# Kernel optimization log

Measured on AMD Instinct MI355X. Metric: run time of the kernel, lower is better.

Reference implementation:

```python
import jax, jax.numpy as jnp
import numpy as np

SCALE = 1.0 / np.sqrt(64.0)  # module hardcodes 64**0.5, independent of d


def setup_inputs() -> dict:
    key = jax.random.key(0)
    k1, k2 = jax.random.split(key)
    x = jax.random.normal(k1, (8, 2048, 512), dtype=jnp.float32)
    kernel = jax.random.normal(k2, (3, 512, 512), dtype=jnp.float32) * 0.02
    return {"x": x, "kernel": kernel}


def reference(x, kernel):
    # x: [b, s, d]; kernel: [3, d, d]
    q = jnp.einsum('bsd,de->bse', x, kernel[0])
    k = jnp.einsum('bsd,de->bse', x, kernel[1])
    v = jnp.einsum('bsd,de->bse', x, kernel[2])
    scores = jnp.einsum('bqd,bkd->bqk', q, k) * SCALE  # [b, s, s]
    attn = jax.nn.softmax(scores, axis=-1)
    return jnp.einsum('bqk,bkd->bqd', attn, v)
```

## Files before the change

### kernel.cpp

```cpp
#include <hip/hip_runtime.h>


typedef unsigned short u16;
typedef unsigned int u32;

using bf16x8 = __attribute__((ext_vector_type(8))) short;
using f32x4  = __attribute__((ext_vector_type(4))) float;
using u16x4  = __attribute__((ext_vector_type(4))) u16;

__device__ __forceinline__ u16 f2bf(float f) {
  u32 u = __float_as_uint(f);
  u32 r = (u + 0x7FFFu + ((u >> 16) & 1u)) >> 16;
  return (u16)r;
}
__device__ __forceinline__ float bf2f(u16 h) {
  return __uint_as_float(((u32)h) << 16);
}

#define GLL16(src, dst)                                                        \
  __builtin_amdgcn_global_load_lds(                                            \
      (const __attribute__((address_space(1))) void*)(src),                    \
      (__attribute__((address_space(3))) void*)(dst), 16, 0, 0)

template <int K>
__device__ __forceinline__ void gemm8p_256x128(
    const u16* __restrict__ A0, const u16* __restrict__ B0,
    u16* lds, f32x4 (&acc)[4][4])
{
  const int tid = threadIdx.x;
  const int w = tid >> 6, l = tid & 63;
  const int wm = w >> 1, wn = w & 1;
  const int fr = l & 15;
  const int laneChunk = ((l >> 4) ^ ((fr >> 1) & 3)) << 3;
  const int laneA = (wm * 64 + fr) * 32 + laneChunk;
  const int laneB = (wn * 64 + fr) * 32 + laneChunk;
  u16* const ldsA = lds;
  u16* const ldsB = lds + 24576;

  const int chunkS = ((tid & 3) ^ ((tid >> 3) & 3)) << 3;
  const int r0 = tid >> 2;
  const u16* const sA0 = A0 + (size_t)r0 * K + chunkS;
  const u16* const sA1 = A0 + (size_t)(r0 + 128) * K + chunkS;
  const u16* const sB0 = B0 + (size_t)r0 * K + chunkS;
  const int dOf = w * 512;

#define PSTAGE_A(j, slot) do {                                                 \
    u16* d_ = ldsA + (slot) * 8192 + dOf;                                      \
    GLL16(sA0 + (j) * 32, d_);                                                 \
    GLL16(sA1 + (j) * 32, d_ + 4096);                                          \
  } while (0)
#define PSTAGE_B(j, slot) do {                                                 \
    u16* d_ = ldsB + (slot) * 4096 + dOf;                                      \
    GLL16(sB0 + (j) * 32, d_);                                                 \
  } while (0)

  PSTAGE_B(0, 0); PSTAGE_A(0, 0);
  PSTAGE_B(1, 1); PSTAGE_A(1, 1);

  constexpr int NS = K / 32;
  int slot = 0;
  for (int j = 0; j < NS; ++j) {
    const int jn = (j + 2 < NS) ? (j + 2) : (NS - 1);
    int slotn = slot + 2; if (slotn >= 3) slotn -= 3;

    asm volatile("s_waitcnt vmcnt(3)\n\ts_barrier" ::: "memory");

    const u16* const Ab = ldsA + slot * 8192;
    const u16* const Bb = ldsB + slot * 4096;
    bf16x8 a[4], b[4];
#pragma unroll
    for (int i = 0; i < 4; ++i) a[i] = *(const bf16x8*)(Ab + laneA + i * 512);
#pragma unroll
    for (int i = 0; i < 4; ++i) b[i] = *(const bf16x8*)(Bb + laneB + i * 512);
    PSTAGE_B(jn, slotn);
    __builtin_amdgcn_s_setprio(1);
#pragma unroll
    for (int mi = 0; mi < 2; ++mi)
#pragma unroll
      for (int nj = 0; nj < 4; ++nj)
        acc[mi][nj] = __builtin_amdgcn_mfma_f32_16x16x32_bf16(a[mi], b[nj], acc[mi][nj], 0, 0, 0);
    __builtin_amdgcn_s_setprio(0);
    PSTAGE_A(jn, slotn);
    __builtin_amdgcn_s_setprio(1);
#pragma unroll
    for (int mi = 2; mi < 4; ++mi)
#pragma unroll
      for (int nj = 0; nj < 4; ++nj)
        acc[mi][nj] = __builtin_amdgcn_mfma_f32_16x16x32_bf16(a[mi], b[nj], acc[mi][nj], 0, 0, 0);
    __builtin_amdgcn_s_setprio(0);

    slot = (slot == 2) ? 0 : slot + 1;
  }
#undef PSTAGE_A
#undef PSTAGE_B
}

template <int K>
__device__ __forceinline__ void gemm8p_256sq(
    const u16* __restrict__ A0, const u16* __restrict__ B0,
    u16* lds, f32x4 (&acc)[8][4])
{
  const int tid = threadIdx.x;
  const int w = tid >> 6, l = tid & 63;
  const int wm = w >> 2, wn = w & 3;
  const int fr = l & 15;
  const int laneChunk = ((l >> 4) ^ ((fr >> 1) & 3)) << 3;
  const int laneA = (wm * 128 + fr) * 32 + laneChunk;
  const int laneB = (wn * 64 + fr) * 32 + laneChunk;
  u16* const ldsA = lds;
  u16* const ldsB = lds + 24576;

  const int chunkS = ((tid & 3) ^ ((tid >> 3) & 3)) << 3;
  const int r0 = tid >> 2;
  const u16* const sA0 = A0 + (size_t)r0 * K + chunkS;
  const u16* const sA1 = A0 + (size_t)(r0 + 128) * K + chunkS;
  const u16* const sB0 = B0 + (size_t)r0 * K + chunkS;
  const u16* const sB1 = B0 + (size_t)(r0 + 128) * K + chunkS;
  const int dOf = w * 512;

#define SSTAGE_A(j, slot) do {                                                 \
    u16* d_ = ldsA + (slot) * 8192 + dOf;                                      \
    GLL16(sA0 + (j) * 32, d_);                                                 \
    GLL16(sA1 + (j) * 32, d_ + 4096);                                          \
  } while (0)
#define SSTAGE_B(j, slot) do {                                                 \
    u16* d_ = ldsB + (slot) * 8192 + dOf;                                      \
    GLL16(sB0 + (j) * 32, d_);                                                 \
    GLL16(sB1 + (j) * 32, d_ + 4096);                                          \
  } while (0)

  SSTAGE_B(0, 0); SSTAGE_A(0, 0);
  SSTAGE_B(1, 1); SSTAGE_A(1, 1);

  constexpr int NS = K / 32;
  int slot = 0;
  for (int j = 0; j < NS; ++j) {
    const int jn = (j + 2 < NS) ? (j + 2) : (NS - 1);
    int slotn = slot + 2; if (slotn >= 3) slotn -= 3;

    asm volatile("s_waitcnt vmcnt(4)\n\ts_barrier" ::: "memory");

    const u16* const Ab = ldsA + slot * 8192;
    const u16* const Bb = ldsB + slot * 8192;
    bf16x8 b[4], a0[4], a1[4];
#pragma unroll
    for (int i = 0; i < 4; ++i) b[i]  = *(const bf16x8*)(Bb + laneB + i * 512);
#pragma unroll
    for (int i = 0; i < 4; ++i) a0[i] = *(const bf16x8*)(Ab + laneA + i * 512);
    SSTAGE_A(jn, slotn);
    __builtin_amdgcn_s_setprio(1);
#pragma unroll
    for (int mi = 0; mi < 4; ++mi)
#pragma unroll
      for (int nj = 0; nj < 4; ++nj)
        acc[mi][nj] = __builtin_amdgcn_mfma_f32_16x16x32_bf16(a0[mi], b[nj], acc[mi][nj], 0, 0, 0);
    __builtin_amdgcn_s_setprio(0);
#pragma unroll
    for (int i = 0; i < 4; ++i) a1[i] = *(const bf16x8*)(Ab + laneA + (4 + i) * 512);
    SSTAGE_B(jn, slotn);
    __builtin_amdgcn_s_setprio(1);
#pragma unroll
    for (int mi = 0; mi < 4; ++mi)
#pragma unroll
      for (int nj = 0; nj < 4; ++nj)
        acc[4 + mi][nj] = __builtin_amdgcn_mfma_f32_16x16x32_bf16(a1[mi], b[nj], acc[4 + mi][nj], 0, 0, 0);
    __builtin_amdgcn_s_setprio(0);

    slot = (slot == 2) ? 0 : slot + 1;
  }
#undef SSTAGE_A
#undef SSTAGE_B
}


__global__ void convert_x_kernel(const float* __restrict__ x, u16* __restrict__ xb) {
  int i = blockIdx.x * 256 + threadIdx.x;
  float4 f = ((const float4*)x)[i];
  u16x4 o = { f2bf(f.x), f2bf(f.y), f2bf(f.z), f2bf(f.w) };
  ((u16x4*)xb)[i] = o;
}

__global__ void convw_kernel(const float* __restrict__ W, u16* __restrict__ wT) {
  __shared__ float tile[32][33];
  const int mtx = blockIdx.z;
  const int e0 = blockIdx.x * 32, d0 = blockIdx.y * 32;
  const int tx = threadIdx.x, ty = threadIdx.y;
  const float* Wm = W + (size_t)mtx * 262144;
#pragma unroll
  for (int i = 0; i < 32; i += 8)
    tile[ty + i][tx] = Wm[(size_t)(d0 + ty + i) * 512 + e0 + tx];
  __syncthreads();
  u16* T = wT + (size_t)mtx * 262144;
#pragma unroll
  for (int i = 0; i < 32; i += 8)
    T[(size_t)(e0 + ty + i) * 512 + d0 + tx] = f2bf(tile[tx][ty + i]);
}

__global__ __launch_bounds__(512, 4) void gemm_qkv128_kernel(
    const u16* __restrict__ xb, const u16* __restrict__ wT,
    u16* __restrict__ qb, u16* __restrict__ kb, u16* __restrict__ vt)
{
  __shared__ __align__(16) u16 lds[36864];
  const int id = blockIdx.x;
  const int xcd = id & 7, t = id >> 3;
  const int n0 = (t % 12) * 128;
  const int m0 = (xcd * 8 + t / 12) * 256;
  f32x4 acc[4][4] = {};
  gemm8p_256x128<512>(xb + (size_t)m0 * 512, wT + (size_t)n0 * 512, lds, acc);

  const int tid = threadIdx.x, w = tid >> 6, l = tid & 63;
  const int wm = w >> 1, wn = w & 1;
  const int which = n0 >> 9;
  const int eb = (n0 & 511) + wn * 64 + (l & 15);
  const int rb = m0 + wm * 64 + (l >> 4) * 4;
  if (which < 2) {
    u16* dst = which ? kb : qb;
#pragma unroll
    for (int mi = 0; mi < 4; ++mi)
#pragma unroll
      for (int nj = 0; nj < 4; ++nj) {
        const int row = rb + mi * 16;
        const int col = eb + nj * 16;
#pragma unroll
        for (int r = 0; r < 4; ++r)
          dst[(size_t)(row + r) * 512 + col] = f2bf(acc[mi][nj][r]);
      }
  } else {
#pragma unroll
    for (int mi = 0; mi < 4; ++mi)
#pragma unroll
      for (int nj = 0; nj < 4; ++nj) {
        const int s = rb + mi * 16;
        const int b = s >> 11, sl = s & 2047;
        const int e = eb + nj * 16;
        u16x4 pk;
#pragma unroll
        for (int r = 0; r < 4; ++r) pk[r] = f2bf(acc[mi][nj][r]);
        *(u16x4*)(vt + (size_t)b * 1048576 + (size_t)e * 2048 + sl) = pk;
      }
  }
}

__global__ __launch_bounds__(512, 2) void gemm_scores256_kernel(
    const u16* __restrict__ qb, const u16* __restrict__ kb, u16* __restrict__ attn)
{
  __shared__ __align__(16) u16 lds[49152];
  const int id = blockIdx.x;
  const int z = id & 7, t = id >> 3;
  const int n0 = (t & 7) * 256;
  const int m0 = (t >> 3) * 256;
  f32x4 acc[8][4] = {};
  gemm8p_256sq<512>(qb + (size_t)z * 1048576 + (size_t)m0 * 512,
                    kb + (size_t)z * 1048576 + (size_t)n0 * 512, lds, acc);

  const int tid = threadIdx.x, w = tid >> 6, l = tid & 63;
  const int wm = w >> 2, wn = w & 3;
  u16* C = attn + (size_t)z * 4194304;
  const int rb = m0 + wm * 128 + (l >> 4) * 4;
  const int cb = n0 + wn * 64 + (l & 15);
#pragma unroll
  for (int mi = 0; mi < 8; ++mi)
#pragma unroll
    for (int nj = 0; nj < 4; ++nj) {
      const int row = rb + mi * 16;
      const int col = cb + nj * 16;
#pragma unroll
      for (int r = 0; r < 4; ++r)
        C[(size_t)(row + r) * 2048 + col] = f2bf(acc[mi][nj][r] * 0.125f);
    }
}

__global__ __launch_bounds__(256) void softmax_kernel(u16* __restrict__ attn) {
  __shared__ float reds[4];
  const size_t row = blockIdx.x;
  u16* p = attn + row * 2048;
  const int t = threadIdx.x, w = t >> 6, l = t & 63;

  uint4 u = ((const uint4*)p)[t];
  u16* us = (u16*)&u;
  float e[8], s = 0.f;
#pragma unroll
  for (int i = 0; i < 8; ++i) { e[i] = __expf(bf2f(us[i])); s += e[i]; }
  for (int off = 32; off >= 1; off >>= 1) s += __shfl_xor(s, off);
  if (l == 0) reds[w] = s;
  __syncthreads();
  s = reds[0] + reds[1] + reds[2] + reds[3];
  const float inv = 1.f / s;

#pragma unroll
  for (int i = 0; i < 8; ++i) us[i] = f2bf(e[i] * inv);
  ((uint4*)p)[t] = u;
}

__global__ __launch_bounds__(512, 4) void gemm_pv8p_kernel(
    const u16* __restrict__ attn, const u16* __restrict__ vt, float* __restrict__ out)
{
  __shared__ __align__(16) u16 lds[36864];
  const int id = blockIdx.x;
  const int z = id & 7;
  const int j = id >> 3;
  const int n0 = (j & 3) * 128;
  const int m0 = (j >> 2) * 256;
  f32x4 acc[4][4] = {};
  gemm8p_256x128<2048>(attn + (size_t)z * 4194304 + (size_t)m0 * 2048,
                       vt + (size_t)z * 1048576 + (size_t)n0 * 2048, lds, acc);

  const int tid = threadIdx.x, w = tid >> 6, l = tid & 63;
  const int wm = w >> 1, wn = w & 1;
  float* C = out + (size_t)z * 1048576;
  const int rb = m0 + wm * 64 + (l >> 4) * 4;
  const int cb = n0 + wn * 64 + (l & 15);
#pragma unroll
  for (int mi = 0; mi < 4; ++mi)
#pragma unroll
    for (int nj = 0; nj < 4; ++nj) {
      const int row = rb + mi * 16;
      const int col = cb + nj * 16;
#pragma unroll
      for (int r = 0; r < 4; ++r)
        C[(size_t)(row + r) * 512 + col] = acc[mi][nj][r];
    }
}

extern "C" void kernel_launch(void* const* d_in, const int* in_sizes, int n_in,
                              void* d_out, int out_size, void* d_ws, size_t ws_size,
                              hipStream_t stream) {
  const float* x = (const float*)d_in[0];
  const float* W = (const float*)d_in[1];
  float* out = (float*)d_out;

  if (ws_size < 117440512) return;
  u16* wsu  = (u16*)d_ws;
  u16* qb   = wsu;
  u16* kb   = qb + 8388608;
  u16* vt   = kb + 8388608;
  u16* attn = vt + 8388608;
  u16* xb   = attn;
  u16* wT   = attn + 8388608;

  convert_x_kernel<<<8192, 256, 0, stream>>>(x, xb);
  convw_kernel<<<dim3(16, 16, 3), dim3(32, 8), 0, stream>>>(W, wT);
  gemm_qkv128_kernel<<<768, 512, 0, stream>>>(xb, wT, qb, kb, vt);
  gemm_scores256_kernel<<<512, 512, 0, stream>>>(qb, kb, attn);
  softmax_kernel<<<16384, 256, 0, stream>>>(attn);
  gemm_pv8p_kernel<<<256, 512, 0, stream>>>(attn, vt, out);
}
```

Before: 143.4 us.

## Fuse softmax into scores and PV GEMMs, add register ping-pong to scores GEMM

```diff
diff --git a/kernel.cpp b/kernel.cpp
--- a/kernel.cpp
+++ b/kernel.cpp
@@ -22,10 +22,10 @@
       (const __attribute__((address_space(1))) void*)(src),                    \
       (__attribute__((address_space(3))) void*)(dst), 16, 0, 0)
 
-template <int K>
+template <int K, bool RSUM>
 __device__ __forceinline__ void gemm8p_256x128(
     const u16* __restrict__ A0, const u16* __restrict__ B0,
-    u16* lds, f32x4 (&acc)[4][4])
+    u16* lds, f32x4 (&acc)[4][4], float* rs)
 {
   const int tid = threadIdx.x;
   const int w = tid >> 6, l = tid & 63;
@@ -89,6 +89,16 @@
         acc[mi][nj] = __builtin_amdgcn_mfma_f32_16x16x32_bf16(a[mi], b[nj], acc[mi][nj], 0, 0, 0);
     __builtin_amdgcn_s_setprio(0);
 
+    if (RSUM) {
+#pragma unroll
+      for (int i = 0; i < 4; ++i) {
+        float s_ = 0.f;
+#pragma unroll
+        for (int e = 0; e < 8; ++e) s_ += bf2f((u16)a[i][e]);
+        rs[i] += s_;
+      }
+    }
+
     slot = (slot == 2) ? 0 : slot + 1;
   }
 #undef PSTAGE_A
@@ -96,7 +106,7 @@
 }
 
 template <int K>
-__device__ __forceinline__ void gemm8p_256sq(
+__device__ __forceinline__ void gemm8p_256sq_pp(
     const u16* __restrict__ A0, const u16* __restrict__ B0,
     u16* lds, f32x4 (&acc)[8][4])
 {
@@ -129,45 +139,58 @@
     GLL16(sB1 + (j) * 32, d_ + 4096);                                          \
   } while (0)
 
+  constexpr int NS = K / 32;
+  bf16x8 bP[4], aP0[4], aP1[4], bQ[4], aQ0[4], aQ1[4];
+
   SSTAGE_B(0, 0); SSTAGE_A(0, 0);
   SSTAGE_B(1, 1); SSTAGE_A(1, 1);
-
-  constexpr int NS = K / 32;
-  int slot = 0;
-  for (int j = 0; j < NS; ++j) {
-    const int jn = (j + 2 < NS) ? (j + 2) : (NS - 1);
-    int slotn = slot + 2; if (slotn >= 3) slotn -= 3;
-
-    asm volatile("s_waitcnt vmcnt(4)\n\ts_barrier" ::: "memory");
-
-    const u16* const Ab = ldsA + slot * 8192;
-    const u16* const Bb = ldsB + slot * 8192;
-    bf16x8 b[4], a0[4], a1[4];
-#pragma unroll
-    for (int i = 0; i < 4; ++i) b[i]  = *(const bf16x8*)(Bb + laneB + i * 512);
-#pragma unroll
-    for (int i = 0; i < 4; ++i) a0[i] = *(const bf16x8*)(Ab + laneA + i * 512);
-    SSTAGE_A(jn, slotn);
-    __builtin_amdgcn_s_setprio(1);
-#pragma unroll
-    for (int mi = 0; mi < 4; ++mi)
-#pragma unroll
-      for (int nj = 0; nj < 4; ++nj)
-        acc[mi][nj] = __builtin_amdgcn_mfma_f32_16x16x32_bf16(a0[mi], b[nj], acc[mi][nj], 0, 0, 0);
-    __builtin_amdgcn_s_setprio(0);
-#pragma unroll
-    for (int i = 0; i < 4; ++i) a1[i] = *(const bf16x8*)(Ab + laneA + (4 + i) * 512);
-    SSTAGE_B(jn, slotn);
-    __builtin_amdgcn_s_setprio(1);
-#pragma unroll
-    for (int mi = 0; mi < 4; ++mi)
-#pragma unroll
-      for (int nj = 0; nj < 4; ++nj)
-        acc[4 + mi][nj] = __builtin_amdgcn_mfma_f32_16x16x32_bf16(a1[mi], b[nj], acc[4 + mi][nj], 0, 0, 0);
-    __builtin_amdgcn_s_setprio(0);
-
-    slot = (slot == 2) ? 0 : slot + 1;
-  }
+  SSTAGE_B(2, 2); SSTAGE_A(2, 2);
+  asm volatile("s_waitcnt vmcnt(8)\n\ts_barrier" ::: "memory");
+#pragma unroll
+  for (int i = 0; i < 4; ++i) bP[i]  = *(const bf16x8*)(ldsB + laneB + i * 512);
+#pragma unroll
+  for (int i = 0; i < 4; ++i) aP0[i] = *(const bf16x8*)(ldsA + laneA + i * 512);
+#pragma unroll
+  for (int i = 0; i < 4; ++i) aP1[i] = *(const bf16x8*)(ldsA + laneA + (4 + i) * 512);
+
+#define SITER(jj, CB, CA0, CA1, NB, NA0, NA1) do {                             \
+    const int js_ = ((jj) + 3 < NS) ? (jj) + 3 : NS - 1;                       \
+    const int sS_ = (jj) % 3;                                                  \
+    const int sR_ = ((jj) + 1) % 3;                                            \
+    asm volatile("s_waitcnt vmcnt(4) lgkmcnt(0)\n\ts_barrier" ::: "memory");   \
+    const u16* const Ab_ = ldsA + sR_ * 8192;                                  \
+    const u16* const Bb_ = ldsB + sR_ * 8192;                                  \
+    _Pragma("unroll")                                                          \
+    for (int i = 0; i < 4; ++i) NB[i]  = *(const bf16x8*)(Bb_ + laneB + i * 512); \
+    _Pragma("unroll")                                                          \
+    for (int i = 0; i < 4; ++i) NA0[i] = *(const bf16x8*)(Ab_ + laneA + i * 512); \
+    SSTAGE_A(js_, sS_);                                                        \
+    __builtin_amdgcn_s_setprio(1);                                             \
+    _Pragma("unroll")                                                          \
+    for (int mi = 0; mi < 4; ++mi)                                             \
+      _Pragma("unroll")                                                        \
+      for (int nj = 0; nj < 4; ++nj)                                           \
+        acc[mi][nj] = __builtin_amdgcn_mfma_f32_16x16x32_bf16(                 \
+            CA0[mi], CB[nj], acc[mi][nj], 0, 0, 0);                            \
+    __builtin_amdgcn_s_setprio(0);                                             \
+    _Pragma("unroll")                                                          \
+    for (int i = 0; i < 4; ++i) NA1[i] = *(const bf16x8*)(Ab_ + laneA + (4 + i) * 512); \
+    SSTAGE_B(js_, sS_);                                                        \
+    __builtin_amdgcn_s_setprio(1);                                             \
+    _Pragma("unroll")                                                          \
+    for (int mi = 0; mi < 4; ++mi)                                             \
+      _Pragma("unroll")                                                        \
+      for (int nj = 0; nj < 4; ++nj)                                           \
+        acc[4 + mi][nj] = __builtin_amdgcn_mfma_f32_16x16x32_bf16(             \
+            CA1[mi], CB[nj], acc[4 + mi][nj], 0, 0, 0);                        \
+    __builtin_amdgcn_s_setprio(0);                                             \
+  } while (0)
+
+  for (int j = 0; j < NS; j += 2) {
+    SITER(j, bP, aP0, aP1, bQ, aQ0, aQ1);
+    SITER(j + 1, bQ, aQ0, aQ1, bP, aP0, aP1);
+  }
+#undef SITER
 #undef SSTAGE_A
 #undef SSTAGE_B
 }
@@ -206,7 +229,7 @@
   const int n0 = (t % 12) * 128;
   const int m0 = (xcd * 8 + t / 12) * 256;
   f32x4 acc[4][4] = {};
-  gemm8p_256x128<512>(xb + (size_t)m0 * 512, wT + (size_t)n0 * 512, lds, acc);
+  gemm8p_256x128<512, false>(xb + (size_t)m0 * 512, wT + (size_t)n0 * 512, lds, acc, nullptr);
 
   const int tid = threadIdx.x, w = tid >> 6, l = tid & 63;
   const int wm = w >> 1, wn = w & 1;
@@ -250,8 +273,8 @@
   const int n0 = (t & 7) * 256;
   const int m0 = (t >> 3) * 256;
   f32x4 acc[8][4] = {};
-  gemm8p_256sq<512>(qb + (size_t)z * 1048576 + (size_t)m0 * 512,
-                    kb + (size_t)z * 1048576 + (size_t)n0 * 512, lds, acc);
+  gemm8p_256sq_pp<512>(qb + (size_t)z * 1048576 + (size_t)m0 * 512,
+                       kb + (size_t)z * 1048576 + (size_t)n0 * 512, lds, acc);
 
   const int tid = threadIdx.x, w = tid >> 6, l = tid & 63;
   const int wm = w >> 2, wn = w & 3;
@@ -266,59 +289,53 @@
       const int col = cb + nj * 16;
 #pragma unroll
       for (int r = 0; r < 4; ++r)
-        C[(size_t)(row + r) * 2048 + col] = f2bf(acc[mi][nj][r] * 0.125f);
+        C[(size_t)(row + r) * 2048 + col] = f2bf(__expf(acc[mi][nj][r] * 0.125f));
     }
-}
-
-__global__ __launch_bounds__(256) void softmax_kernel(u16* __restrict__ attn) {
-  __shared__ float reds[4];
-  const size_t row = blockIdx.x;
-  u16* p = attn + row * 2048;
-  const int t = threadIdx.x, w = t >> 6, l = t & 63;
-
-  uint4 u = ((const uint4*)p)[t];
-  u16* us = (u16*)&u;
-  float e[8], s = 0.f;
-#pragma unroll
-  for (int i = 0; i < 8; ++i) { e[i] = __expf(bf2f(us[i])); s += e[i]; }
-  for (int off = 32; off >= 1; off >>= 1) s += __shfl_xor(s, off);
-  if (l == 0) reds[w] = s;
-  __syncthreads();
-  s = reds[0] + reds[1] + reds[2] + reds[3];
-  const float inv = 1.f / s;
-
-#pragma unroll
-  for (int i = 0; i < 8; ++i) us[i] = f2bf(e[i] * inv);
-  ((uint4*)p)[t] = u;
 }
 
 __global__ __launch_bounds__(512, 4) void gemm_pv8p_kernel(
     const u16* __restrict__ attn, const u16* __restrict__ vt, float* __restrict__ out)
 {
   __shared__ __align__(16) u16 lds[36864];
+  __shared__ float rowsumLDS[256];
   const int id = blockIdx.x;
   const int z = id & 7;
   const int j = id >> 3;
   const int n0 = (j & 3) * 128;
   const int m0 = (j >> 2) * 256;
   f32x4 acc[4][4] = {};
-  gemm8p_256x128<2048>(attn + (size_t)z * 4194304 + (size_t)m0 * 2048,
-                       vt + (size_t)z * 1048576 + (size_t)n0 * 2048, lds, acc);
+  float rs[4] = {0.f, 0.f, 0.f, 0.f};
+  gemm8p_256x128<2048, true>(attn + (size_t)z * 4194304 + (size_t)m0 * 2048,
+                             vt + (size_t)z * 1048576 + (size_t)n0 * 2048, lds, acc, rs);
 
   const int tid = threadIdx.x, w = tid >> 6, l = tid & 63;
   const int wm = w >> 1, wn = w & 1;
+
+  __syncthreads();
+#pragma unroll
+  for (int mi = 0; mi < 4; ++mi) {
+    rs[mi] += __shfl_xor(rs[mi], 16);
+    rs[mi] += __shfl_xor(rs[mi], 32);
+  }
+  if ((l >> 4) == 0) {
+#pragma unroll
+    for (int mi = 0; mi < 4; ++mi)
+      rowsumLDS[wm * 64 + mi * 16 + l] = rs[mi];
+  }
+  __syncthreads();
+
   float* C = out + (size_t)z * 1048576;
   const int rb = m0 + wm * 64 + (l >> 4) * 4;
   const int cb = n0 + wn * 64 + (l & 15);
 #pragma unroll
   for (int mi = 0; mi < 4; ++mi)
 #pragma unroll
-    for (int nj = 0; nj < 4; ++nj) {
-      const int row = rb + mi * 16;
-      const int col = cb + nj * 16;
-#pragma unroll
-      for (int r = 0; r < 4; ++r)
-        C[(size_t)(row + r) * 512 + col] = acc[mi][nj][r];
+    for (int r = 0; r < 4; ++r) {
+      const float inv = 1.f / rowsumLDS[wm * 64 + mi * 16 + (l >> 4) * 4 + r];
+      const int row = rb + mi * 16 + r;
+#pragma unroll
+      for (int nj = 0; nj < 4; ++nj)
+        C[(size_t)row * 512 + cb + nj * 16] = acc[mi][nj][r] * inv;
     }
 }
 
@@ -342,6 +359,5 @@
   convw_kernel<<<dim3(16, 16, 3), dim3(32, 8), 0, stream>>>(W, wT);
   gemm_qkv128_kernel<<<768, 512, 0, stream>>>(xb, wT, qb, kb, vt);
   gemm_scores256_kernel<<<512, 512, 0, stream>>>(qb, kb, attn);
-  softmax_kernel<<<16384, 256, 0, stream>>>(attn);
   gemm_pv8p_kernel<<<256, 512, 0, stream>>>(attn, vt, out);
 }
```

New measurement: 132.0 us. -7.9%, faster.
